# Kernel tuning notes

Measured on AMD Instinct MI355X. Metric: run time of the kernel, lower is better.

The kernel has to match this reference:

```python
import jax, jax.numpy as jnp
import numpy as np

B, F, D = 1024, 256, 64  # batch, featureNumb, featureDim


def setup_inputs() -> dict:
    key = jax.random.key(0)
    k1, k2, k3, k4 = jax.random.split(key, 4)
    feature = jax.random.normal(k1, (B, F, D), dtype=jnp.float32)
    indicator = jax.random.normal(k2, (F, D), dtype=jnp.float32)
    # QKVTransformV2(n, D, D): n stacked DxD linear maps of the indicator
    W_qk = jax.random.normal(k3, (2, D, D), dtype=jnp.float32) / np.float32(np.sqrt(D))
    W_qkv = jax.random.normal(k4, (3, D, D), dtype=jnp.float32) / np.float32(np.sqrt(D))
    return {"feature": feature, "indicator": indicator, "W_qk": W_qk, "W_qkv": W_qkv}


def reference(feature, indicator, W_qk, W_qkv):
    d = indicator.shape[-1]
    scale = jnp.asarray(1.0 / np.sqrt(d), feature.dtype)

    # --- gate branch: QKTrans + DotWeight + LTE (straight-through hard threshold) ---
    trans = jnp.einsum('fd,nde->nfe', indicator, W_qk)            # [2,F,D]
    gate_logits = jnp.einsum('id,jd->ij', trans[0], trans[1]) * scale  # [F,F]
    gate = (gate_logits > 0).astype(feature.dtype)                # LTE forward: hard 0/1 gate

    # --- QKV branch, fused form of the rank-1 outer products ---
    # Original: QKV_outer[t,i,j] = qkv[t,i] (x) qkv[t,j]  (DxD rank-1)
    #           input[b,t,i,j,:] = feature[b,i] @ QKV_outer[t,i,j]
    #                            = (feature[b,i] . qkv[t,i]) * qkv[t,j]
    qkv = jnp.einsum('fd,nde->nfe', indicator, W_qkv)             # [3,F,D]
    s = jnp.einsum('bfd,nfd->nbf', feature, qkv)                  # s[t,b,i] = feature[b,i].qkv[t,i]

    # score[b,i,j] = input[b,0,i,j,:] . input[b,1,j,i,:]
    #              = s[0,b,i] * s[1,b,j] * (qkv[1,i] . qkv[0,j])
    cross = jnp.einsum('id,jd->ij', qkv[1], qkv[0])               # [F,F]
    score = s[0][:, :, None] * s[1][:, None, :] * cross[None]     # [B,F,F]
    scoreHat = score * gate[None]                                 # [B,F,F]

    # output[b,i,:] = sum_j scoreHat[b,i,j] * value[b,i,j,:]
    #               = s[2,b,i] * sum_j scoreHat[b,i,j] * qkv[2,j,:]
    out = s[2][:, :, None] * jnp.einsum('bij,jd->bid', scoreHat, qkv[2])  # [B,F,D]
    return out
```

## Files before the change

kernel.cpp:

```cpp
#include <hip/hip_runtime.h>
#include <stdint.h>

#define B 1024
#define F 256
#define D 64

typedef __attribute__((ext_vector_type(8))) short short8;
typedef __attribute__((ext_vector_type(4))) float f32x4;

__device__ __forceinline__ short f2bf(float f) {
    unsigned u = __builtin_bit_cast(unsigned, f);
    u += 0x7fff + ((u >> 16) & 1);
    return (short)(u >> 16);
}
__device__ __forceinline__ float bf2f(short s) {
    unsigned u = ((unsigned)(unsigned short)s) << 16;
    return __builtin_bit_cast(float, u);
}
__device__ __forceinline__ unsigned pk_bf16(float a, float b) {
    unsigned ua = __builtin_bit_cast(unsigned, a) + 0x8000u;
    unsigned ub = __builtin_bit_cast(unsigned, b) + 0x8000u;
    return __builtin_amdgcn_perm(ub, ua, 0x07060302u);
}


__global__ void precompute_trans(const float* __restrict__ indicator,
                                 const float* __restrict__ W_qk,
                                 const float* __restrict__ W_qkv,
                                 float* __restrict__ trans,
                                 float* __restrict__ qkv) {
    int idx = blockIdx.x * blockDim.x + threadIdx.x;
    int n   = idx / (F * D);
    int rem = idx - n * (F * D);
    int f   = rem / D;
    int e   = rem - f * D;
    const float* W = (n < 2) ? (W_qk + n * D * D) : (W_qkv + (n - 2) * D * D);
    const float* ind = indicator + f * D;
    float acc = 0.f;
#pragma unroll 8
    for (int d = 0; d < D; ++d) acc += ind[d] * W[d * D + e];
    if (n < 2) trans[n * F * D + f * D + e] = acc;
    else       qkv[(n - 2) * F * D + f * D + e] = acc;
}

__global__ __launch_bounds__(256) void compute_Mt(const float* __restrict__ trans,
                                                  const float* __restrict__ qkv,
                                                  short* __restrict__ At,
                                                  short* __restrict__ q2K) {
    int j = blockIdx.x;
    int i = threadIdx.x;
    const float4* t0 = (const float4*)(trans + i * D);
    const float4* t1 = (const float4*)(trans + F * D + j * D);
    const float4* q1 = (const float4*)(qkv + F * D + i * D);
    const float4* q0 = (const float4*)(qkv + j * D);
    float d0 = 0.f, d1 = 0.f;
#pragma unroll
    for (int k = 0; k < D / 4; ++k) {
        float4 a = t0[k], b = t1[k], c = q1[k], e = q0[k];
        d0 += a.x * b.x + a.y * b.y + a.z * b.z + a.w * b.w;
        d1 += c.x * e.x + c.y * e.y + c.z * e.z + c.w * e.w;
    }
    float v = (d0 > 0.f) ? d1 : 0.f;
    At[((j >> 5) * F + i) * 32 + (j & 31)] = f2bf(v);
    if (j < D) q2K[((i >> 5) * D + j) * 32 + (i & 31)] = f2bf(qkv[2 * F * D + i * D + j]);
}

__global__ __launch_bounds__(256) void compute_s(const float* __restrict__ feature,
                                                 const float* __restrict__ qkv,
                                                 float* __restrict__ g,
                                                 short* __restrict__ s1b) {
    int gid = blockIdx.x * 256 + threadIdx.x;
    int row = gid >> 4;
    int l   = gid & 15;
    int f   = row & (F - 1);
    float4 fv = ((const float4*)(feature + (size_t)row * D))[l];
    float4 q0 = ((const float4*)(qkv + f * D))[l];
    float4 q1 = ((const float4*)(qkv + F * D + f * D))[l];
    float4 q2 = ((const float4*)(qkv + 2 * F * D + f * D))[l];
    float p0 = fv.x * q0.x + fv.y * q0.y + fv.z * q0.z + fv.w * q0.w;
    float p1 = fv.x * q1.x + fv.y * q1.y + fv.z * q1.z + fv.w * q1.w;
    float p2 = fv.x * q2.x + fv.y * q2.y + fv.z * q2.z + fv.w * q2.w;
#pragma unroll
    for (int m = 1; m < 16; m <<= 1) {
        p0 += __shfl_xor(p0, m, 64);
        p1 += __shfl_xor(p1, m, 64);
        p2 += __shfl_xor(p2, m, 64);
    }
    if (l == 0) {
        g[row]   = p0 * p2;
        s1b[row] = f2bf(p1);
    }
}

__global__ __launch_bounds__(256) void main_mfma(const short* __restrict__ At,
                                                 const short* __restrict__ q2K,
                                                 const short* __restrict__ s1b,
                                                 const float* __restrict__ g,
                                                 float* __restrict__ out) {
    int blk = blockIdx.x;
    int ih  = blk & 1;
    int bp  = blk >> 1;
    int b0  = bp * 2;
    int i0  = ih * 128;

    int tid  = threadIdx.x;
    int wave = tid >> 6;
    int lane = tid & 63;
    int wr   = wave >> 1, wc = wave & 1;
    int l16  = lane & 15;
    int lq   = lane >> 4;
    int b    = b0 + wc;

    f32x4 acc[4][4];
#pragma unroll
    for (int mt = 0; mt < 4; ++mt)
#pragma unroll
        for (int nt = 0; nt < 4; ++nt) acc[mt][nt] = (f32x4){0.f, 0.f, 0.f, 0.f};

    for (int jt = 0; jt < F / 32; ++jt) {
        int kq = lq * 8;
        short8 sv = *(const short8*)(s1b + b * F + jt * 32 + kq);
        float sf[8];
#pragma unroll
        for (int e = 0; e < 8; ++e) sf[e] = bf2f(sv[e]);

        short8 af[4];
#pragma unroll
        for (int mt = 0; mt < 4; ++mt) {
            int i = i0 + wr * 64 + mt * 16 + l16;
            af[mt] = *(const short8*)(At + (jt * F + i) * 32 + kq);
        }
        short8 bf[4];
#pragma unroll
        for (int nt = 0; nt < 4; ++nt) {
            int d = nt * 16 + l16;
            short8 qv = *(const short8*)(q2K + (jt * D + d) * 32 + kq);
            int4 packed;
            packed.x = pk_bf16(bf2f(qv[0]) * sf[0], bf2f(qv[1]) * sf[1]);
            packed.y = pk_bf16(bf2f(qv[2]) * sf[2], bf2f(qv[3]) * sf[3]);
            packed.z = pk_bf16(bf2f(qv[4]) * sf[4], bf2f(qv[5]) * sf[5]);
            packed.w = pk_bf16(bf2f(qv[6]) * sf[6], bf2f(qv[7]) * sf[7]);
            bf[nt] = __builtin_bit_cast(short8, packed);
        }
#pragma unroll
        for (int mt = 0; mt < 4; ++mt)
#pragma unroll
            for (int nt = 0; nt < 4; ++nt)
                acc[mt][nt] = __builtin_amdgcn_mfma_f32_16x16x32_bf16(
                    af[mt], bf[nt], acc[mt][nt], 0, 0, 0);
    }

#pragma unroll
    for (int mt = 0; mt < 4; ++mt) {
#pragma unroll
        for (int r = 0; r < 4; ++r) {
            int i_loc = wr * 64 + mt * 16 + lq * 4 + r;
            float gg = g[b * F + i0 + i_loc];
            float* orow = out + ((size_t)(b * F + i0 + i_loc)) * D;
#pragma unroll
            for (int nt = 0; nt < 4; ++nt)
                orow[nt * 16 + l16] = gg * acc[mt][nt][r];
        }
    }
}

extern "C" void kernel_launch(void* const* d_in, const int* in_sizes, int n_in,
                              void* d_out, int out_size, void* d_ws, size_t ws_size,
                              hipStream_t stream) {
    const float* feature   = (const float*)d_in[0];
    const float* indicator = (const float*)d_in[1];
    const float* W_qk      = (const float*)d_in[2];
    const float* W_qkv     = (const float*)d_in[3];
    float* out = (float*)d_out;

    float* ws    = (float*)d_ws;
    float* trans = ws;
    float* qkv   = trans + 2 * F * D;
    float* g     = qkv + 3 * F * D;
    short* At    = (short*)(g + B * F);
    short* q2K   = At + F * F;
    short* s1b   = q2K + (F / 32) * D * 32;

    hipLaunchKernelGGL(precompute_trans, dim3((5 * F * D) / 256), dim3(256), 0,
                       stream, indicator, W_qk, W_qkv, trans, qkv);
    hipLaunchKernelGGL(compute_Mt, dim3(F), dim3(F), 0, stream, trans, qkv, At, q2K);
    hipLaunchKernelGGL(compute_s, dim3(B * F * 16 / 256), dim3(256), 0, stream,
                       feature, qkv, g, s1b);
    hipLaunchKernelGGL(main_mfma, dim3(B), dim3(256), 0, stream, At, q2K,
                       s1b, g, out);
}
```

Measured before the change: 148.4 us.

## Fuse per-row projection reduction into MFMA kernel with shared-memory staging

Merges the compute_s kernel into the main MFMA kernel. Each block now computes s0/s1/s2 for its two batch rows into shared memory, which removes one launch and the global round-trip of g and s1b. Each block also covers all 256 output rows instead of 128, so each wave holds 8x4 accumulator tiles and loads A fragments inside the mt loop. This raises register pressure and halves the grid to 512 blocks, which may reduce occupancy.

```diff
diff --git a/kernel.cpp b/kernel.cpp
--- a/kernel.cpp
+++ b/kernel.cpp
@@ -65,72 +65,75 @@
     if (j < D) q2K[((i >> 5) * D + j) * 32 + (i & 31)] = f2bf(qkv[2 * F * D + i * D + j]);
 }
 
-__global__ __launch_bounds__(256) void compute_s(const float* __restrict__ feature,
-                                                 const float* __restrict__ qkv,
-                                                 float* __restrict__ g,
-                                                 short* __restrict__ s1b) {
-    int gid = blockIdx.x * 256 + threadIdx.x;
-    int row = gid >> 4;
-    int l   = gid & 15;
-    int f   = row & (F - 1);
-    float4 fv = ((const float4*)(feature + (size_t)row * D))[l];
-    float4 q0 = ((const float4*)(qkv + f * D))[l];
-    float4 q1 = ((const float4*)(qkv + F * D + f * D))[l];
-    float4 q2 = ((const float4*)(qkv + 2 * F * D + f * D))[l];
-    float p0 = fv.x * q0.x + fv.y * q0.y + fv.z * q0.z + fv.w * q0.w;
-    float p1 = fv.x * q1.x + fv.y * q1.y + fv.z * q1.z + fv.w * q1.w;
-    float p2 = fv.x * q2.x + fv.y * q2.y + fv.z * q2.z + fv.w * q2.w;
+__global__ __launch_bounds__(256, 2) void fused_main(const float* __restrict__ feature,
+                                                     const float* __restrict__ qkv,
+                                                     const short* __restrict__ At,
+                                                     const short* __restrict__ q2K,
+                                                     float* __restrict__ out) {
+    int bp = blockIdx.x;
+    int b0 = bp * 2;
+    int tid = threadIdx.x;
+
+    __shared__ __align__(16) short s1L[2 * F];
+    __shared__ float gL[2 * F];
+
+    {
+        int rg = tid >> 4;
+        int l  = tid & 15;
+#pragma unroll 4
+        for (int p = 0; p < 16; ++p) {
+            int f = p * 16 + rg;
+            float4 fv0 = ((const float4*)(feature + ((size_t)(b0 * F + f)) * D))[l];
+            float4 fv1 = ((const float4*)(feature + ((size_t)((b0 + 1) * F + f)) * D))[l];
+            float4 q0 = ((const float4*)(qkv + f * D))[l];
+            float4 q1 = ((const float4*)(qkv + F * D + f * D))[l];
+            float4 q2 = ((const float4*)(qkv + 2 * F * D + f * D))[l];
+            float a00 = fv0.x * q0.x + fv0.y * q0.y + fv0.z * q0.z + fv0.w * q0.w;
+            float a01 = fv0.x * q1.x + fv0.y * q1.y + fv0.z * q1.z + fv0.w * q1.w;
+            float a02 = fv0.x * q2.x + fv0.y * q2.y + fv0.z * q2.z + fv0.w * q2.w;
+            float a10 = fv1.x * q0.x + fv1.y * q0.y + fv1.z * q0.z + fv1.w * q0.w;
+            float a11 = fv1.x * q1.x + fv1.y * q1.y + fv1.z * q1.z + fv1.w * q1.w;
+            float a12 = fv1.x * q2.x + fv1.y * q2.y + fv1.z * q2.z + fv1.w * q2.w;
 #pragma unroll
-    for (int m = 1; m < 16; m <<= 1) {
-        p0 += __shfl_xor(p0, m, 64);
-        p1 += __shfl_xor(p1, m, 64);
-        p2 += __shfl_xor(p2, m, 64);
+            for (int m = 1; m < 16; m <<= 1) {
+                a00 += __shfl_xor(a00, m, 64);
+                a01 += __shfl_xor(a01, m, 64);
+                a02 += __shfl_xor(a02, m, 64);
+                a10 += __shfl_xor(a10, m, 64);
+                a11 += __shfl_xor(a11, m, 64);
+                a12 += __shfl_xor(a12, m, 64);
+            }
+            if (l == 0) {
+                gL[f]       = a00 * a02;
+                gL[F + f]   = a10 * a12;
+                s1L[f]      = f2bf(a01);
+                s1L[F + f]  = f2bf(a11);
+            }
+        }
     }
-    if (l == 0) {
-        g[row]   = p0 * p2;
-        s1b[row] = f2bf(p1);
-    }
-}
+    __syncthreads();
 
-__global__ __launch_bounds__(256) void main_mfma(const short* __restrict__ At,
-                                                 const short* __restrict__ q2K,
-                                                 const short* __restrict__ s1b,
-                                                 const float* __restrict__ g,
-                                                 float* __restrict__ out) {
-    int blk = blockIdx.x;
-    int ih  = blk & 1;
-    int bp  = blk >> 1;
-    int b0  = bp * 2;
-    int i0  = ih * 128;
-
-    int tid  = threadIdx.x;
     int wave = tid >> 6;
     int lane = tid & 63;
     int wr   = wave >> 1, wc = wave & 1;
     int l16  = lane & 15;
     int lq   = lane >> 4;
+    int kq   = lq * 8;
     int b    = b0 + wc;
 
-    f32x4 acc[4][4];
+    f32x4 acc[8][4];
 #pragma unroll
-    for (int mt = 0; mt < 4; ++mt)
+    for (int mt = 0; mt < 8; ++mt)
 #pragma unroll
         for (int nt = 0; nt < 4; ++nt) acc[mt][nt] = (f32x4){0.f, 0.f, 0.f, 0.f};
 
     for (int jt = 0; jt < F / 32; ++jt) {
-        int kq = lq * 8;
-        short8 sv = *(const short8*)(s1b + b * F + jt * 32 + kq);
+        short8 sv = *(const short8*)(s1L + wc * F + jt * 32 + kq);
         float sf[8];
 #pragma unroll
         for (int e = 0; e < 8; ++e) sf[e] = bf2f(sv[e]);
 
-        short8 af[4];
-#pragma unroll
-        for (int mt = 0; mt < 4; ++mt) {
-            int i = i0 + wr * 64 + mt * 16 + l16;
-            af[mt] = *(const short8*)(At + (jt * F + i) * 32 + kq);
-        }
-        short8 bf[4];
+        short8 bfr[4];
 #pragma unroll
         for (int nt = 0; nt < 4; ++nt) {
             int d = nt * 16 + l16;
@@ -140,23 +143,26 @@
             packed.y = pk_bf16(bf2f(qv[2]) * sf[2], bf2f(qv[3]) * sf[3]);
             packed.z = pk_bf16(bf2f(qv[4]) * sf[4], bf2f(qv[5]) * sf[5]);
             packed.w = pk_bf16(bf2f(qv[6]) * sf[6], bf2f(qv[7]) * sf[7]);
-            bf[nt] = __builtin_bit_cast(short8, packed);
+            bfr[nt] = __builtin_bit_cast(short8, packed);
         }
 #pragma unroll
-        for (int mt = 0; mt < 4; ++mt)
+        for (int mt = 0; mt < 8; ++mt) {
+            int i = wr * 128 + mt * 16 + l16;
+            short8 af = *(const short8*)(At + ((size_t)jt * F + i) * 32 + kq);
 #pragma unroll
             for (int nt = 0; nt < 4; ++nt)
                 acc[mt][nt] = __builtin_amdgcn_mfma_f32_16x16x32_bf16(
-                    af[mt], bf[nt], acc[mt][nt], 0, 0, 0);
+                    af, bfr[nt], acc[mt][nt], 0, 0, 0);
+        }
     }
 
 #pragma unroll
-    for (int mt = 0; mt < 4; ++mt) {
+    for (int mt = 0; mt < 8; ++mt) {
 #pragma unroll
         for (int r = 0; r < 4; ++r) {
-            int i_loc = wr * 64 + mt * 16 + lq * 4 + r;
-            float gg = g[b * F + i0 + i_loc];
-            float* orow = out + ((size_t)(b * F + i0 + i_loc)) * D;
+            int i = wr * 128 + mt * 16 + lq * 4 + r;
+            float gg = gL[wc * F + i];
+            float* orow = out + ((size_t)(b * F + i)) * D;
 #pragma unroll
             for (int nt = 0; nt < 4; ++nt)
                 orow[nt * 16 + l16] = gg * acc[mt][nt][r];
@@ -176,16 +182,12 @@
     float* ws    = (float*)d_ws;
     float* trans = ws;
     float* qkv   = trans + 2 * F * D;
-    float* g     = qkv + 3 * F * D;
-    short* At    = (short*)(g + B * F);
+    short* At    = (short*)(qkv + 3 * F * D);
     short* q2K   = At + F * F;
-    short* s1b   = q2K + (F / 32) * D * 32;
 
     hipLaunchKernelGGL(precompute_trans, dim3((5 * F * D) / 256), dim3(256), 0,
                        stream, indicator, W_qk, W_qkv, trans, qkv);
     hipLaunchKernelGGL(compute_Mt, dim3(F), dim3(F), 0, stream, trans, qkv, At, q2K);
-    hipLaunchKernelGGL(compute_s, dim3(B * F * 16 / 256), dim3(256), 0, stream,
-                       feature, qkv, g, s1b);
-    hipLaunchKernelGGL(main_mfma, dim3(B), dim3(256), 0, stream, At, q2K,
-                       s1b, g, out);
+    hipLaunchKernelGGL(fused_main, dim3(B / 2), dim3(256), 0, stream,
+                       feature, qkv, At, q2K, out);
 }
```

Measured after the change: 143.1 us. 1.04x faster.
